# Performance work log

Hardware: AMD Instinct MI355X
Metric: run time of the kernel (lower is better)

The kernel has to match this reference:

```python
import jax, jax.numpy as jnp
import numpy as np

B, S, E, D = 8, 2048, 1024, 512

def setup_inputs() -> dict:
    key = jax.random.key(0)
    ks = jax.random.split(key, 7)
    scale = 1.0 / np.sqrt(E)
    return {
        "X": jax.random.normal(ks[0], (B, S, E), dtype=jnp.float32),
        "lam": jnp.float32(0.8),
        "W_q": jax.random.uniform(ks[1], (E, 2 * D), jnp.float32, -scale, scale),
        "b_q": jax.random.uniform(ks[2], (2 * D,), jnp.float32, -scale, scale),
        "W_k": jax.random.uniform(ks[3], (E, 2 * D), jnp.float32, -scale, scale),
        "b_k": jax.random.uniform(ks[4], (2 * D,), jnp.float32, -scale, scale),
        "W_v": jax.random.uniform(ks[5], (E, D), jnp.float32, -scale, scale),
        "b_v": jax.random.uniform(ks[6], (D,), jnp.float32, -scale, scale),
    }

def reference(X, lam, W_q, b_q, W_k, b_k, W_v, b_v):
    # Projections
    Q = X @ W_q + b_q          # [B, S, 2D]
    K = X @ W_k + b_k          # [B, S, 2D]
    V = X @ W_v + b_v          # [B, S, D]
    Q1, Q2 = Q[..., :D], Q[..., D:]
    K1, K2 = K[..., :D], K[..., D:]
    s = 1.0 / np.sqrt(D)
    A1 = jnp.einsum('bqd,bkd->bqk', Q1, K1) * s  # [B, S, S]
    A2 = jnp.einsum('bqd,bkd->bqk', Q2, K2) * s
    P = jax.nn.softmax(A1, axis=-1) - lam * jax.nn.softmax(A2, axis=-1)
    return jnp.einsum('bqk,bkd->bqd', P, V)      # [B, S, D]
```

## Files before the change

kernel.cpp:

```cpp
#include <hip/hip_runtime.h>


typedef unsigned short u16;
typedef short    bf16x8 __attribute__((ext_vector_type(8)));
typedef unsigned short u16x8 __attribute__((ext_vector_type(8)));
typedef unsigned short u16x4 __attribute__((ext_vector_type(4)));
typedef float    f32x4  __attribute__((ext_vector_type(4)));

typedef __attribute__((address_space(3))) unsigned int       lds_uint;
typedef __attribute__((address_space(1))) const unsigned int gl_uint;

__device__ __forceinline__ void glds16(const void* g, void* l) {
  __builtin_amdgcn_global_load_lds((gl_uint*)g, (lds_uint*)l, 16, 0, 0);
}

__device__ __forceinline__ u16 to_bf16(float f) {
  unsigned u = __float_as_uint(f);
  return (u16)((u + 0x7FFFu + ((u >> 16) & 1u)) >> 16);
}
__device__ __forceinline__ float b2f(u16 h) {
  return __uint_as_float(((unsigned)h) << 16);
}


__global__ void cvt_x(const float4* __restrict__ in, u16x4* __restrict__ out, int n4) {
  int i = blockIdx.x * 256 + threadIdx.x;
  if (i >= n4) return;
  float4 v = in[i];
  u16x4 o;
  o[0] = to_bf16(v.x); o[1] = to_bf16(v.y); o[2] = to_bf16(v.z); o[3] = to_bf16(v.w);
  out[i] = o;
}

__global__ void transpose_cvt(const float* __restrict__ in, u16* __restrict__ out,
                              int R, int C) {
  __shared__ float t[64][65];
  int c0 = blockIdx.x * 64, r0 = blockIdx.y * 64;
  int tx = threadIdx.x, ty = threadIdx.y;
  #pragma unroll
  for (int i = 0; i < 64; i += 4)
    t[ty + i][tx] = in[(long)(r0 + ty + i) * C + c0 + tx];
  __syncthreads();
  #pragma unroll
  for (int i = 0; i < 64; i += 4)
    out[(long)(c0 + ty + i) * R + r0 + tx] = to_bf16(t[tx][ty + i]);
}

__global__ void concat2(const float* __restrict__ a, const float* __restrict__ b,
                        float* __restrict__ o, int n) {
  int i = blockIdx.x * 256 + threadIdx.x;
  if (i < n) o[i] = a[i];
  else if (i < 2 * n) o[i] = b[i - n];
}

__device__ __forceinline__ void swizzle_tiles(int& tm, int& tn) {
  int nx = gridDim.x;
  int lin = blockIdx.y * nx + blockIdx.x;
  int span = nx * 4;
  int group = lin / span;
  int ing = lin % span;
  tm = group * 4 + (ing & 3);
  tn = ing >> 2;
}

__global__ __launch_bounds__(256, 4) void gemm_nt(
    const u16* __restrict__ A, int lda,
    const u16* __restrict__ B, int ldb,
    u16* __restrict__ C1, u16* __restrict__ C2, int splitN, int ldc,
    int Kd, float scale,
    const float* __restrict__ bias, int biasMode)
{
  __shared__ u16 SM[2][8192];
  u16* As = SM[0];
  u16* Bs = SM[1];

  int tid = threadIdx.x;
  int wave = tid >> 6, lane = tid & 63;
  int quad = lane >> 4, ln = lane & 15;
  int wm = wave >> 1, wn = wave & 1;
  int tm, tn;
  swizzle_tiles(tm, tn);
  int c8 = lane >> 3, ml = lane & 7;

  const f32x4 fz = {0.f, 0.f, 0.f, 0.f};
  f32x4 acc[4][4];
  #pragma unroll
  for (int i = 0; i < 4; i++)
    #pragma unroll
    for (int j = 0; j < 4; j++) acc[i][j] = fz;

  const u16* Abase = A + (long)(tm * 128 + ml) * lda + c8 * 8;
  const u16* Bbase = B + (long)(tn * 128 + ml) * ldb + c8 * 8;

  for (int kt = 0; kt < Kd; kt += 64) {
    __syncthreads();
    #pragma unroll
    for (int i = 0; i < 4; i++) {
      int mg = wave * 4 + i;
      glds16(Abase + (long)mg * 8 * lda + kt, &As[mg * 512]);
      glds16(Bbase + (long)mg * 8 * ldb + kt, &Bs[mg * 512]);
    }
    __syncthreads();
    #pragma unroll
    for (int ks = 0; ks < 2; ks++) {
      bf16x8 af[4], bfr[4];
      int c = ks * 4 + quad;
      #pragma unroll
      for (int mt = 0; mt < 4; mt++) {
        int m = wm * 64 + mt * 16 + ln;
        af[mt] = *(const bf16x8*)&As[((m >> 3) * 64 + c * 8 + (m & 7)) * 8];
      }
      #pragma unroll
      for (int nt = 0; nt < 4; nt++) {
        int n = wn * 64 + nt * 16 + ln;
        bfr[nt] = *(const bf16x8*)&Bs[((n >> 3) * 64 + c * 8 + (n & 7)) * 8];
      }
      #pragma unroll
      for (int mt = 0; mt < 4; mt++)
        #pragma unroll
        for (int nt = 0; nt < 4; nt++)
          acc[mt][nt] = __builtin_amdgcn_mfma_f32_16x16x32_bf16(af[mt], bfr[nt], acc[mt][nt], 0, 0, 0);
    }
  }

  int rowBase = tm * 128 + wm * 64;
  int colBase = tn * 128 + wn * 64;
  u16* Cw = C1; int outCol = colBase;
  if (colBase >= splitN) { Cw = C2; outCol = colBase - splitN; }
  u16* eb = &SM[0][0] + wave * 4096;

  __syncthreads();
  #pragma unroll
  for (int mt = 0; mt < 4; mt++) {
    #pragma unroll
    for (int nt = 0; nt < 4; nt++) {
      int colL = nt * 16 + ln;
      float bcol = (biasMode == 1) ? bias[colBase + colL] : 0.f;
      #pragma unroll
      for (int r = 0; r < 4; r++) {
        int rowL = mt * 16 + quad * 4 + r;
        float brow = (biasMode == 2) ? bias[rowBase + rowL] : 0.f;
        float v = acc[mt][nt][r] * scale + bcol + brow;
        eb[rowL * 64 + (((colL >> 3) ^ (rowL & 7)) << 3) + (colL & 7)] = to_bf16(v);
      }
    }
  }
  {
    int row = lane;
    long gr = (long)(rowBase + row) * ldc + outCol;
    #pragma unroll
    for (int c = 0; c < 8; c++) {
      u16x8 ch = *(const u16x8*)&eb[row * 64 + ((c ^ (row & 7)) << 3)];
      *(u16x8*)&Cw[gr + c * 8] = ch;
    }
  }
}


__global__ __launch_bounds__(512, 2) void gemm_s256p(
    const u16* __restrict__ Q, const u16* __restrict__ K,
    u16* __restrict__ E1, u16* __restrict__ E2,
    float* __restrict__ statsP, float scale)
{
  __shared__ u16 SM[73728];

  int bz = blockIdx.z >> 1, half = blockIdx.z & 1;
  const u16* A = Q + (long)bz * 2097152 + half * 512;
  const u16* B = K + (long)bz * 2097152 + half * 512;
  u16* Ed = (half ? E2 : E1) + (long)bz * 4194304;
  float* sp = statsP + (long)blockIdx.z * 65536;

  int tn = blockIdx.x;
  int tmg = blockIdx.y;
  int tid = threadIdx.x;
  int wave = tid >> 6, lane = tid & 63, quad = lane >> 4, ln = lane & 15;
  int wm = wave >> 2, wn = wave & 3;
  int dr = ((lane >> 5) << 3) + (lane & 7);
  int cg = (lane >> 3) & 3;

  const f32x4 fz = {0.f, 0.f, 0.f, 0.f};
  f32x4 acc[8][4];
  #pragma unroll
  for (int i = 0; i < 8; i++)
    #pragma unroll
    for (int j = 0; j < 4; j++) acc[i][j] = fz;

  const u16* Abase = A + (long)(tmg * 1024 + wave * 32 + dr) * 1024 + cg * 8;
  const u16* Bbase = B + (long)(tn * 256 + wave * 32 + dr) * 1024 + cg * 8;
  u16* ldsA0 = SM;
  u16* ldsB0 = SM + 16384;
  u16* eb = SM + 40960 + wave * 4096;

  glds16(Abase,                ldsA0 + wave * 1024);
  glds16(Abase + 16 * 1024,    ldsA0 + wave * 1024 + 512);
  glds16(Bbase,                ldsB0 + wave * 1024);
  glds16(Bbase + 16 * 1024,    ldsB0 + wave * 1024 + 512);
  glds16(Bbase + 32,           ldsB0 + 8192 + wave * 1024);
  glds16(Bbase + 16 * 1024 + 32, ldsB0 + 8192 + wave * 1024 + 512);
  asm volatile("s_waitcnt vmcnt(2)" ::: "memory");
  __builtin_amdgcn_s_barrier();
  __builtin_amdgcn_sched_barrier(0);

  for (int T = 0; T < 64; T++) {
    const u16* Ar = ldsA0 + (T & 1) * 8192;
    const u16* Br = ldsB0 + (T % 3) * 8192;

    {
      int Ta = (T + 1 < 64) ? T + 1 : 63;
      long roff = (long)((Ta >> 4) * 256) * 1024 + ((Ta & 15) << 5);
      u16* dA = ldsA0 + (Ta & 1) * 8192 + wave * 1024;
      glds16(Abase + roff,             dA);
      glds16(Abase + roff + 16 * 1024, dA + 512);
      int Tb = (T + 2 < 64) ? T + 2 : 63;
      int ktB = (Tb & 15) << 5;
      u16* dB = ldsB0 + (Tb % 3) * 8192 + wave * 1024;
      glds16(Bbase + ktB,             dB);
      glds16(Bbase + ktB + 16 * 1024, dB + 512);
    }
    __builtin_amdgcn_sched_barrier(0);

    bf16x8 bfr[4];
    #pragma unroll
    for (int nt = 0; nt < 4; nt++) {
      int n = wn * 64 + nt * 16 + ln;
      bfr[nt] = *(const bf16x8*)(Br + ((n >> 3) * 32 + quad * 8 + (n & 7)) * 8);
    }
    #pragma unroll
    for (int g = 0; g < 8; g++) {
      int m = wm * 128 + g * 16 + ln;
      bf16x8 af = *(const bf16x8*)(Ar + ((m >> 3) * 32 + quad * 8 + (m & 7)) * 8);
      #pragma unroll
      for (int nt = 0; nt < 4; nt++)
        acc[g][nt] = __builtin_amdgcn_mfma_f32_16x16x32_bf16(af, bfr[nt], acc[g][nt], 0, 0, 0);
    }

    asm volatile("s_waitcnt vmcnt(2)" ::: "memory");
    __builtin_amdgcn_s_barrier();
    __builtin_amdgcn_sched_barrier(0);

    if ((T & 15) == 15) {
      int sub = T >> 4;
      int rowBaseW = (tmg * 4 + sub) * 256 + wm * 128;
      int colBase = tn * 256 + wn * 64;
      int kb = tn * 4 + wn;
      #pragma unroll
      for (int h = 0; h < 2; h++) {
        #pragma unroll
        for (int mt = 0; mt < 4; mt++) {
          #pragma unroll
          for (int nt = 0; nt < 4; nt++) {
            int colL = nt * 16 + ln;
            #pragma unroll
            for (int r = 0; r < 4; r++) {
              int rowL = mt * 16 + quad * 4 + r;
              eb[rowL * 64 + (((colL >> 3) ^ (rowL & 7)) << 3) + (colL & 7)] =
                  to_bf16(__expf(acc[h * 4 + mt][nt][r] * scale));
            }
          }
        }
        {
          int row = lane;
          u16x8 ch[8];
          #pragma unroll
          for (int c = 0; c < 8; c++)
            ch[c] = *(const u16x8*)&eb[row * 64 + ((c ^ (row & 7)) << 3)];
          u16* Ep = Ed + (long)(rowBaseW + h * 64 + row) * 2048 + colBase;
          #pragma unroll
          for (int c = 0; c < 8; c++)
            *(u16x8*)&Ep[c * 8] = ch[c];
          float L = 0.f;
          #pragma unroll
          for (int c = 0; c < 8; c++)
            #pragma unroll
            for (int j = 0; j < 8; j++) L += b2f(ch[c][j]);
          sp[(rowBaseW + h * 64 + row) * 32 + kb] = L;
        }
      }
      #pragma unroll
      for (int i = 0; i < 8; i++)
        #pragma unroll
        for (int j = 0; j < 4; j++) acc[i][j] = fz;
    }
  }
  asm volatile("s_waitcnt vmcnt(0)" ::: "memory");
}

__global__ __launch_bounds__(512, 2) void gemm_nt256p(
    const u16* __restrict__ A, const u16* __restrict__ B,
    u16* __restrict__ C1, u16* __restrict__ C2, int splitN, int ldc,
    float scale, const float* __restrict__ bias, int biasMode)
{
  __shared__ u16 SM[73728];

  int tn = blockIdx.x;
  int tmg = blockIdx.y;
  int tid = threadIdx.x;
  int wave = tid >> 6, lane = tid & 63, quad = lane >> 4, ln = lane & 15;
  int wm = wave >> 2, wn = wave & 3;
  int dr = ((lane >> 5) << 3) + (lane & 7);
  int cg = (lane >> 3) & 3;

  const f32x4 fz = {0.f, 0.f, 0.f, 0.f};
  f32x4 acc[8][4];
  #pragma unroll
  for (int i = 0; i < 8; i++)
    #pragma unroll
    for (int j = 0; j < 4; j++) acc[i][j] = fz;

  const u16* Abase = A + (long)(tmg * 512 + wave * 32 + dr) * 1024 + cg * 8;
  const u16* Bbase = B + (long)(tn * 256 + wave * 32 + dr) * 1024 + cg * 8;
  u16* ldsA0 = SM;
  u16* ldsB0 = SM + 16384;
  u16* eb = SM + 40960 + wave * 4096;

  glds16(Abase,                  ldsA0 + wave * 1024);
  glds16(Abase + 16 * 1024,      ldsA0 + wave * 1024 + 512);
  glds16(Bbase,                  ldsB0 + wave * 1024);
  glds16(Bbase + 16 * 1024,      ldsB0 + wave * 1024 + 512);
  glds16(Bbase + 32,             ldsB0 + 8192 + wave * 1024);
  glds16(Bbase + 16 * 1024 + 32, ldsB0 + 8192 + wave * 1024 + 512);
  asm volatile("s_waitcnt vmcnt(2)" ::: "memory");
  __builtin_amdgcn_s_barrier();
  __builtin_amdgcn_sched_barrier(0);

  for (int T = 0; T < 64; T++) {
    const u16* Ar = ldsA0 + (T & 1) * 8192;
    const u16* Br = ldsB0 + (T % 3) * 8192;

    {
      int Ta = (T + 1 < 64) ? T + 1 : 63;
      long roff = (long)((Ta >> 5) * 256) * 1024 + ((Ta & 31) << 5);
      u16* dA = ldsA0 + (Ta & 1) * 8192 + wave * 1024;
      glds16(Abase + roff,             dA);
      glds16(Abase + roff + 16 * 1024, dA + 512);
      int Tb = (T + 2 < 64) ? T + 2 : 63;
      int ktB = (Tb & 31) << 5;
      u16* dB = ldsB0 + (Tb % 3) * 8192 + wave * 1024;
      glds16(Bbase + ktB,             dB);
      glds16(Bbase + ktB + 16 * 1024, dB + 512);
    }
    __builtin_amdgcn_sched_barrier(0);

    bf16x8 bfr[4];
    #pragma unroll
    for (int nt = 0; nt < 4; nt++) {
      int n = wn * 64 + nt * 16 + ln;
      bfr[nt] = *(const bf16x8*)(Br + ((n >> 3) * 32 + quad * 8 + (n & 7)) * 8);
    }
    #pragma unroll
    for (int g = 0; g < 8; g++) {
      int m = wm * 128 + g * 16 + ln;
      bf16x8 af = *(const bf16x8*)(Ar + ((m >> 3) * 32 + quad * 8 + (m & 7)) * 8);
      #pragma unroll
      for (int nt = 0; nt < 4; nt++)
        acc[g][nt] = __builtin_amdgcn_mfma_f32_16x16x32_bf16(af, bfr[nt], acc[g][nt], 0, 0, 0);
    }

    asm volatile("s_waitcnt vmcnt(2)" ::: "memory");
    __builtin_amdgcn_s_barrier();
    __builtin_amdgcn_sched_barrier(0);

    if ((T & 31) == 31) {
      int sub = T >> 5;
      int rowBaseW = (tmg * 2 + sub) * 256 + wm * 128;
      int colBase = tn * 256 + wn * 64;
      u16* Cw = C1; int outCol = colBase;
      if (colBase >= splitN) { Cw = C2; outCol = colBase - splitN; }
      #pragma unroll
      for (int h = 0; h < 2; h++) {
        #pragma unroll
        for (int mt = 0; mt < 4; mt++) {
          #pragma unroll
          for (int nt = 0; nt < 4; nt++) {
            int colL = nt * 16 + ln;
            float bcol = (biasMode == 1) ? bias[colBase + colL] : 0.f;
            #pragma unroll
            for (int r = 0; r < 4; r++) {
              int rowL = mt * 16 + quad * 4 + r;
              float brow = (biasMode == 2) ? bias[rowBaseW + h * 64 + rowL] : 0.f;
              float v = acc[h * 4 + mt][nt][r] * scale + bcol + brow;
              eb[rowL * 64 + (((colL >> 3) ^ (rowL & 7)) << 3) + (colL & 7)] = to_bf16(v);
            }
          }
        }
        {
          int row = lane;
          long gr = (long)(rowBaseW + h * 64 + row) * ldc + outCol;
          #pragma unroll
          for (int c = 0; c < 8; c++) {
            u16x8 ch = *(const u16x8*)&eb[row * 64 + ((c ^ (row & 7)) << 3)];
            *(u16x8*)&Cw[gr + c * 8] = ch;
          }
        }
      }
      #pragma unroll
      for (int i = 0; i < 8; i++)
        #pragma unroll
        for (int j = 0; j < 4; j++) acc[i][j] = fz;
    }
  }
  asm volatile("s_waitcnt vmcnt(0)" ::: "memory");
}

__global__ void stats_reduce(const float* __restrict__ sp, float* __restrict__ so,
                             const float* __restrict__ lamPtr) {
  int gid = blockIdx.x * 256 + threadIdx.x;
  const float* p = sp + (long)gid * 32;
  float L = 0.f;
  #pragma unroll
  for (int kb = 0; kb < 32; kb++) L += p[kb];
  int half = (gid >> 11) & 1;
  so[gid] = (half ? lamPtr[0] : 1.0f) / L;
}

__global__ __launch_bounds__(512, 2) void apply_pv(
    const u16* __restrict__ E1, const u16* __restrict__ E2,
    const u16* __restrict__ VT, const float* __restrict__ inv,
    float* __restrict__ Out)
{
  __shared__ u16 Vs[2][32768];
  __shared__ u16 Pb[2][4096];
  __shared__ float i1s[64], i2s[64];

  const int NT = 32;
  int b = blockIdx.x & 7, qt = blockIdx.x >> 3;
  int q0 = qt * 64;
  int tid = threadIdx.x;
  int wave = tid >> 6, lane = tid & 63, quad = lane >> 4, ln = lane & 15;
  int c8 = lane >> 3, ml = lane & 7;
  int r = tid >> 3, cg8 = tid & 7;

  const u16* e1p = E1 + ((long)b * 2048 + q0 + r) * 2048 + cg8 * 8;
  const u16* e2p = E2 + ((long)b * 2048 + q0 + r) * 2048 + cg8 * 8;
  const u16* Vbase = VT + (long)b * 2048;
  int pw = (r >> 3) * 512 + cg8 * 64 + (r & 7) * 8;

  const f32x4 fz = {0.f, 0.f, 0.f, 0.f};
  f32x4 acc[4][4];
  #pragma unroll
  for (int i = 0; i < 4; i++)
    #pragma unroll
    for (int j = 0; j < 4; j++) acc[i][j] = fz;

  if (tid < 64)       i1s[tid]       = inv[(long)(b * 2 + 0) * 2048 + q0 + tid];
  else if (tid < 128) i2s[tid - 64]  = inv[(long)(b * 2 + 1) * 2048 + q0 + (tid - 64)];
  u16x8 a1 = *(const u16x8*)(e1p);
  u16x8 a2 = *(const u16x8*)(e2p);
  __builtin_amdgcn_sched_barrier(0);
  #pragma unroll
  for (int i = 0; i < 8; i++) {
    int dg = wave * 8 + i;
    glds16(Vbase + (long)(dg * 8 + ml) * 16384 + c8 * 8, &Vs[0][dg * 512]);
  }
  __builtin_amdgcn_sched_barrier(0);
  asm volatile("s_waitcnt lgkmcnt(0)" ::: "memory");
  __builtin_amdgcn_s_barrier();
  __builtin_amdgcn_sched_barrier(0);
  float i1 = i1s[r], i2 = i2s[r];
  {
    u16x8 o;
    #pragma unroll
    for (int j = 0; j < 8; j++)
      o[j] = to_bf16(b2f(a1[j]) * i1 - b2f(a2[j]) * i2);
    *(u16x8*)&Pb[0][pw] = o;
  }
  a1 = *(const u16x8*)(e1p + 64);
  a2 = *(const u16x8*)(e2p + 64);
  __builtin_amdgcn_sched_barrier(0);
  asm volatile("s_waitcnt lgkmcnt(0)" ::: "memory");
  asm volatile("s_waitcnt vmcnt(2)" ::: "memory");
  __builtin_amdgcn_sched_barrier(0);
  __builtin_amdgcn_s_barrier();
  __builtin_amdgcn_sched_barrier(0);

  for (int t = 0; t < NT; t++) {
    const int p = t & 1;
    const u16* Vr = &Vs[p][0];
    const u16* Pr = &Pb[p][0];
    u16* Vw = &Vs[p ^ 1][0];
    u16* Pw = &Pb[p ^ 1][0];
    int ktv = ((t + 1 < NT) ? (t + 1) : (NT - 1)) << 6;
    int kte = ((t + 2 < NT) ? (t + 2) : (NT - 1)) << 6;
    bf16x8 vf[2][4];

    #pragma unroll
    for (int q = 0; q < 4; q++) {
      bf16x8 pf[2];
      #pragma unroll
      for (int ks = 0; ks < 2; ks++) {
        int m = q * 16 + ln;
        pf[ks] = *(const bf16x8*)&Pr[((m >> 3) * 64 + (ks * 4 + quad) * 8 + (m & 7)) * 8];
      }
      if (q == 0) {
        #pragma unroll
        for (int ks = 0; ks < 2; ks++)
          #pragma unroll
          for (int nt = 0; nt < 4; nt++) {
            int d = wave * 64 + nt * 16 + ln;
            vf[ks][nt] = *(const bf16x8*)&Vr[((d >> 3) * 64 + (ks * 4 + quad) * 8 + (d & 7)) * 8];
          }
      }
      #pragma unroll
      for (int i = 0; i < 2; i++) {
        int dg = wave * 8 + q * 2 + i;
        glds16(Vbase + (long)(dg * 8 + ml) * 16384 + ktv + c8 * 8, Vw + dg * 512);
      }
      if (q == 3) {
        __builtin_amdgcn_sched_barrier(0);
        u16x8 o;
        #pragma unroll
        for (int j = 0; j < 8; j++)
          o[j] = to_bf16(b2f(a1[j]) * i1 - b2f(a2[j]) * i2);
        *(u16x8*)&Pw[pw] = o;
        a1 = *(const u16x8*)(e1p + kte);
        a2 = *(const u16x8*)(e2p + kte);
      }
      __builtin_amdgcn_sched_barrier(0);
      __builtin_amdgcn_s_barrier();
      asm volatile("s_waitcnt lgkmcnt(0)" ::: "memory");
      __builtin_amdgcn_sched_barrier(0);
      __builtin_amdgcn_s_setprio(1);
      #pragma unroll
      for (int ks = 0; ks < 2; ks++)
        #pragma unroll
        for (int nt = 0; nt < 4; nt++)
          acc[q][nt] = __builtin_amdgcn_mfma_f32_16x16x32_bf16(pf[ks], vf[ks][nt], acc[q][nt], 0, 0, 0);
      __builtin_amdgcn_s_setprio(0);
      __builtin_amdgcn_sched_barrier(0);
      if (q == 3) asm volatile("s_waitcnt vmcnt(2)" ::: "memory");
      __builtin_amdgcn_s_barrier();
      __builtin_amdgcn_sched_barrier(0);
    }
  }

  #pragma unroll
  for (int mt = 0; mt < 4; mt++)
    #pragma unroll
    for (int nt = 0; nt < 4; nt++)
      #pragma unroll
      for (int r2 = 0; r2 < 4; r2++)
        Out[((long)b * 2048 + q0 + mt * 16 + quad * 4 + r2) * 512 + wave * 64 + nt * 16 + ln] =
            acc[mt][nt][r2];
}


extern "C" void kernel_launch(void* const* d_in, const int* in_sizes, int n_in,
                              void* d_out, int out_size, void* d_ws, size_t ws_size,
                              hipStream_t stream)
{
  const float* X   = (const float*)d_in[0];
  const float* lam = (const float*)d_in[1];
  const float* Wq  = (const float*)d_in[2];
  const float* bq  = (const float*)d_in[3];
  const float* Wk  = (const float*)d_in[4];
  const float* bk  = (const float*)d_in[5];
  const float* Wv  = (const float*)d_in[6];
  const float* bv  = (const float*)d_in[7];
  float* Out = (float*)d_out;
  char* ws = (char*)d_ws;

  u16*  WqkT   = (u16*)(ws + 0);
  u16*  WvT    = (u16*)(ws + 4194304);
  float* bqk   = (float*)(ws + 5242880);
  u16*  Qb     = (u16*)(ws + 6291456);
  u16*  Kb     = (u16*)(ws + 39845888);
  u16*  VTb    = (u16*)(ws + 73400320);
  u16*  Xb     = (u16*)(ws + 90177536);
  u16*  E1     = (u16*)(ws + 90177536);
  u16*  E2     = (u16*)(ws + 157286400);
  float* statsP= (float*)(ws + 224395264);
  float* invD  = (float*)(ws + 228589568);

  cvt_x<<<16384, 256, 0, stream>>>((const float4*)X, (u16x4*)Xb, 4194304);
  transpose_cvt<<<dim3(16, 16), dim3(64, 4), 0, stream>>>(Wq, WqkT, 1024, 1024);
  transpose_cvt<<<dim3(16, 16), dim3(64, 4), 0, stream>>>(Wk, WqkT + 1024 * 1024, 1024, 1024);
  transpose_cvt<<<dim3(8, 16),  dim3(64, 4), 0, stream>>>(Wv, WvT, 1024, 512);
  concat2<<<8, 256, 0, stream>>>(bq, bk, bqk, 1024);

  gemm_nt256p<<<dim3(8, 32), 512, 0, stream>>>(Xb, WqkT, Qb, Kb, 1024, 1024,
                                               1.0f, bqk, 1);
  gemm_nt<<<dim3(128, 4), 256, 0, stream>>>(WvT, 1024, Xb, 1024,
                                            VTb, VTb, 1 << 30, 16384,
                                            1024, 1.0f, bv, 2);

  const float s = 0.044194173824159216f;
  gemm_s256p<<<dim3(8, 2, 16), 512, 0, stream>>>(Qb, Kb, E1, E2, statsP, s);

  stats_reduce<<<128, 256, 0, stream>>>(statsP, invD, lam);
  apply_pv<<<256, 512, 0, stream>>>(E1, E2, VTb, invD, Out);
}
```

Before: 474.9 us.

## Shrink QK and score GEMM tiles to 128x128 with grouped block swizzle

The Q/K projection GEMM and the score GEMM move from 512-thread blocks with 256x256 tiles and a triple-buffered B pipeline to 256-thread blocks with 128x128 tiles, double buffering and 40KB LDS. Blocks are launched as a flat grid remapped into groups of eight panels for L2 locality. The aim is more resident blocks per CU and more blocks in the grid for better load balance. In exchange each tile gets less operand reuse and has to wait on vmcnt(0) every step, removing the prefetch depth. The epilogue now writes 16-row chunks and uses shuffles to reduce the row sums.

```diff
diff --git a/kernel.cpp b/kernel.cpp
--- a/kernel.cpp
+++ b/kernel.cpp
@@ -157,65 +157,67 @@
 }
 
 
-__global__ __launch_bounds__(512, 2) void gemm_s256p(
+__global__ __launch_bounds__(256, 4) void gemm_s128p(
     const u16* __restrict__ Q, const u16* __restrict__ K,
     u16* __restrict__ E1, u16* __restrict__ E2,
     float* __restrict__ statsP, float scale)
 {
-  __shared__ u16 SM[73728];
-
-  int bz = blockIdx.z >> 1, half = blockIdx.z & 1;
+  __shared__ u16 SM[20480];
+
+  int blk = blockIdx.x;
+  int g = blk & 7, r = blk >> 3;
+  int pan = g + 8 * (r >> 4);
+  int tn = r & 15;
+  int tmg = pan & 3, z = pan >> 2;
+  int bz = z >> 1, half = z & 1;
+
   const u16* A = Q + (long)bz * 2097152 + half * 512;
   const u16* B = K + (long)bz * 2097152 + half * 512;
   u16* Ed = (half ? E2 : E1) + (long)bz * 4194304;
-  float* sp = statsP + (long)blockIdx.z * 65536;
-
-  int tn = blockIdx.x;
-  int tmg = blockIdx.y;
+  float* sp = statsP + (long)z * 65536;
+
   int tid = threadIdx.x;
   int wave = tid >> 6, lane = tid & 63, quad = lane >> 4, ln = lane & 15;
-  int wm = wave >> 2, wn = wave & 3;
+  int wm = wave >> 1, wn = wave & 1;
   int dr = ((lane >> 5) << 3) + (lane & 7);
   int cg = (lane >> 3) & 3;
 
   const f32x4 fz = {0.f, 0.f, 0.f, 0.f};
-  f32x4 acc[8][4];
-  #pragma unroll
-  for (int i = 0; i < 8; i++)
+  f32x4 acc[4][4];
+  #pragma unroll
+  for (int i = 0; i < 4; i++)
     #pragma unroll
     for (int j = 0; j < 4; j++) acc[i][j] = fz;
 
-  const u16* Abase = A + (long)(tmg * 1024 + wave * 32 + dr) * 1024 + cg * 8;
-  const u16* Bbase = B + (long)(tn * 256 + wave * 32 + dr) * 1024 + cg * 8;
-  u16* ldsA0 = SM;
-  u16* ldsB0 = SM + 16384;
-  u16* eb = SM + 40960 + wave * 4096;
-
-  glds16(Abase,                ldsA0 + wave * 1024);
-  glds16(Abase + 16 * 1024,    ldsA0 + wave * 1024 + 512);
-  glds16(Bbase,                ldsB0 + wave * 1024);
-  glds16(Bbase + 16 * 1024,    ldsB0 + wave * 1024 + 512);
-  glds16(Bbase + 32,           ldsB0 + 8192 + wave * 1024);
-  glds16(Bbase + 16 * 1024 + 32, ldsB0 + 8192 + wave * 1024 + 512);
-  asm volatile("s_waitcnt vmcnt(2)" ::: "memory");
+  const u16* Ab = A + (long)(tmg * 512 + dr) * 1024 + cg * 8;
+  const u16* Bb = B + (long)(tn * 128 + dr) * 1024 + cg * 8;
+  u16* eb = SM + 16384 + wave * 1024;
+
+  #pragma unroll
+  for (int i = 0; i < 2; i++) {
+    int g16 = wave * 2 + i;
+    glds16(Ab + (long)(g16 * 16) * 1024, SM + g16 * 512);
+    glds16(Bb + (long)(g16 * 16) * 1024, SM + 8192 + g16 * 512);
+  }
+  asm volatile("s_waitcnt vmcnt(0)" ::: "memory");
   __builtin_amdgcn_s_barrier();
   __builtin_amdgcn_sched_barrier(0);
 
   for (int T = 0; T < 64; T++) {
-    const u16* Ar = ldsA0 + (T & 1) * 8192;
-    const u16* Br = ldsB0 + (T % 3) * 8192;
+    const u16* Ar = SM + (T & 1) * 4096;
+    const u16* Br = SM + 8192 + (T & 1) * 4096;
 
     {
-      int Ta = (T + 1 < 64) ? T + 1 : 63;
-      long roff = (long)((Ta >> 4) * 256) * 1024 + ((Ta & 15) << 5);
-      u16* dA = ldsA0 + (Ta & 1) * 8192 + wave * 1024;
-      glds16(Abase + roff,             dA);
-      glds16(Abase + roff + 16 * 1024, dA + 512);
-      int Tb = (T + 2 < 64) ? T + 2 : 63;
-      int ktB = (Tb & 15) << 5;
-      u16* dB = ldsB0 + (Tb % 3) * 8192 + wave * 1024;
-      glds16(Bbase + ktB,             dB);
-      glds16(Bbase + ktB + 16 * 1024, dB + 512);
+      int Tn = (T + 1 < 64) ? T + 1 : 63;
+      int sub_n = Tn >> 4, kt_n = (Tn & 15) << 5;
+      u16* dA = SM + (Tn & 1) * 4096;
+      u16* dB = SM + 8192 + (Tn & 1) * 4096;
+      #pragma unroll
+      for (int i = 0; i < 2; i++) {
+        int g16 = wave * 2 + i;
+        glds16(Ab + (long)(sub_n * 128 + g16 * 16) * 1024 + kt_n, dA + g16 * 512);
+        glds16(Bb + (long)(g16 * 16) * 1024 + kt_n,               dB + g16 * 512);
+      }
     }
     __builtin_amdgcn_sched_barrier(0);
 
@@ -223,121 +225,119 @@
     #pragma unroll
     for (int nt = 0; nt < 4; nt++) {
       int n = wn * 64 + nt * 16 + ln;
-      bfr[nt] = *(const bf16x8*)(Br + ((n >> 3) * 32 + quad * 8 + (n & 7)) * 8);
-    }
-    #pragma unroll
-    for (int g = 0; g < 8; g++) {
-      int m = wm * 128 + g * 16 + ln;
-      bf16x8 af = *(const bf16x8*)(Ar + ((m >> 3) * 32 + quad * 8 + (m & 7)) * 8);
+      bfr[nt] = *(const bf16x8*)(Br + (n >> 3) * 256 + quad * 64 + (n & 7) * 8);
+    }
+    #pragma unroll
+    for (int mt = 0; mt < 4; mt++) {
+      int m = wm * 64 + mt * 16 + ln;
+      bf16x8 af = *(const bf16x8*)(Ar + (m >> 3) * 256 + quad * 64 + (m & 7) * 8);
       #pragma unroll
       for (int nt = 0; nt < 4; nt++)
-        acc[g][nt] = __builtin_amdgcn_mfma_f32_16x16x32_bf16(af, bfr[nt], acc[g][nt], 0, 0, 0);
-    }
-
-    asm volatile("s_waitcnt vmcnt(2)" ::: "memory");
+        acc[mt][nt] = __builtin_amdgcn_mfma_f32_16x16x32_bf16(af, bfr[nt], acc[mt][nt], 0, 0, 0);
+    }
+
+    asm volatile("s_waitcnt vmcnt(0)" ::: "memory");
     __builtin_amdgcn_s_barrier();
     __builtin_amdgcn_sched_barrier(0);
 
     if ((T & 15) == 15) {
       int sub = T >> 4;
-      int rowBaseW = (tmg * 4 + sub) * 256 + wm * 128;
-      int colBase = tn * 256 + wn * 64;
-      int kb = tn * 4 + wn;
-      #pragma unroll
-      for (int h = 0; h < 2; h++) {
-        #pragma unroll
-        for (int mt = 0; mt < 4; mt++) {
+      int rowB = tmg * 512 + sub * 128 + wm * 64;
+      int colB = tn * 128 + wn * 64;
+      int kb = tn * 2 + wn;
+      #pragma unroll
+      for (int c2 = 0; c2 < 4; c2++) {
+        #pragma unroll
+        for (int nt = 0; nt < 4; nt++) {
+          int colL = nt * 16 + ln;
           #pragma unroll
-          for (int nt = 0; nt < 4; nt++) {
-            int colL = nt * 16 + ln;
-            #pragma unroll
-            for (int r = 0; r < 4; r++) {
-              int rowL = mt * 16 + quad * 4 + r;
-              eb[rowL * 64 + (((colL >> 3) ^ (rowL & 7)) << 3) + (colL & 7)] =
-                  to_bf16(__expf(acc[h * 4 + mt][nt][r] * scale));
-            }
+          for (int rr = 0; rr < 4; rr++) {
+            int rowL = quad * 4 + rr;
+            eb[rowL * 64 + (((colL >> 3) ^ (rowL & 7)) << 3) + (colL & 7)] =
+                to_bf16(__expf(acc[c2][nt][rr] * scale));
           }
         }
         {
-          int row = lane;
-          u16x8 ch[8];
+          int row = lane & 15, hf = lane >> 4;
+          float L = 0.f;
+          u16x8 ch[2];
           #pragma unroll
-          for (int c = 0; c < 8; c++)
-            ch[c] = *(const u16x8*)&eb[row * 64 + ((c ^ (row & 7)) << 3)];
-          u16* Ep = Ed + (long)(rowBaseW + h * 64 + row) * 2048 + colBase;
-          #pragma unroll
-          for (int c = 0; c < 8; c++)
-            *(u16x8*)&Ep[c * 8] = ch[c];
-          float L = 0.f;
-          #pragma unroll
-          for (int c = 0; c < 8; c++)
+          for (int cc = 0; cc < 2; cc++) {
+            int c = hf * 2 + cc;
+            ch[cc] = *(const u16x8*)&eb[row * 64 + ((c ^ (row & 7)) << 3)];
             #pragma unroll
-            for (int j = 0; j < 8; j++) L += b2f(ch[c][j]);
-          sp[(rowBaseW + h * 64 + row) * 32 + kb] = L;
+            for (int j = 0; j < 8; j++) L += b2f(ch[cc][j]);
+          }
+          u16* Ep = Ed + (long)(rowB + c2 * 16 + row) * 2048 + colB + hf * 16;
+          *(u16x8*)&Ep[0] = ch[0];
+          *(u16x8*)&Ep[8] = ch[1];
+          L += __shfl_xor(L, 16);
+          L += __shfl_xor(L, 32);
+          if (hf == 0)
+            sp[(rowB + c2 * 16 + row) * 32 + kb] = L;
         }
-      }
-      #pragma unroll
-      for (int i = 0; i < 8; i++)
-        #pragma unroll
-        for (int j = 0; j < 4; j++) acc[i][j] = fz;
+        #pragma unroll
+        for (int j = 0; j < 4; j++) acc[c2][j] = fz;
+      }
     }
   }
   asm volatile("s_waitcnt vmcnt(0)" ::: "memory");
 }
 
-__global__ __launch_bounds__(512, 2) void gemm_nt256p(
+__global__ __launch_bounds__(256, 4) void gemm_nt128p(
     const u16* __restrict__ A, const u16* __restrict__ B,
     u16* __restrict__ C1, u16* __restrict__ C2, int splitN, int ldc,
-    float scale, const float* __restrict__ bias, int biasMode)
+    const float* __restrict__ bias)
 {
-  __shared__ u16 SM[73728];
-
-  int tn = blockIdx.x;
-  int tmg = blockIdx.y;
+  __shared__ u16 SM[20480];
+
+  int blk = blockIdx.x;
+  int g = blk & 7, r = blk >> 3;
+  int pan = g + 8 * (r >> 4);
+  int tn = r & 15;
+
   int tid = threadIdx.x;
   int wave = tid >> 6, lane = tid & 63, quad = lane >> 4, ln = lane & 15;
-  int wm = wave >> 2, wn = wave & 3;
+  int wm = wave >> 1, wn = wave & 1;
   int dr = ((lane >> 5) << 3) + (lane & 7);
   int cg = (lane >> 3) & 3;
 
   const f32x4 fz = {0.f, 0.f, 0.f, 0.f};
-  f32x4 acc[8][4];
-  #pragma unroll
-  for (int i = 0; i < 8; i++)
+  f32x4 acc[4][4];
+  #pragma unroll
+  for (int i = 0; i < 4; i++)
     #pragma unroll
     for (int j = 0; j < 4; j++) acc[i][j] = fz;
 
-  const u16* Abase = A + (long)(tmg * 512 + wave * 32 + dr) * 1024 + cg * 8;
-  const u16* Bbase = B + (long)(tn * 256 + wave * 32 + dr) * 1024 + cg * 8;
-  u16* ldsA0 = SM;
-  u16* ldsB0 = SM + 16384;
-  u16* eb = SM + 40960 + wave * 4096;
-
-  glds16(Abase,                  ldsA0 + wave * 1024);
-  glds16(Abase + 16 * 1024,      ldsA0 + wave * 1024 + 512);
-  glds16(Bbase,                  ldsB0 + wave * 1024);
-  glds16(Bbase + 16 * 1024,      ldsB0 + wave * 1024 + 512);
-  glds16(Bbase + 32,             ldsB0 + 8192 + wave * 1024);
-  glds16(Bbase + 16 * 1024 + 32, ldsB0 + 8192 + wave * 1024 + 512);
-  asm volatile("s_waitcnt vmcnt(2)" ::: "memory");
+  const u16* Ab = A + (long)(pan * 256 + dr) * 1024 + cg * 8;
+  const u16* Bb = B + (long)(tn * 128 + dr) * 1024 + cg * 8;
+  u16* eb = SM + 16384 + wave * 1024;
+
+  #pragma unroll
+  for (int i = 0; i < 2; i++) {
+    int g16 = wave * 2 + i;
+    glds16(Ab + (long)(g16 * 16) * 1024, SM + g16 * 512);
+    glds16(Bb + (long)(g16 * 16) * 1024, SM + 8192 + g16 * 512);
+  }
+  asm volatile("s_waitcnt vmcnt(0)" ::: "memory");
   __builtin_amdgcn_s_barrier();
   __builtin_amdgcn_sched_barrier(0);
 
   for (int T = 0; T < 64; T++) {
-    const u16* Ar = ldsA0 + (T & 1) * 8192;
-    const u16* Br = ldsB0 + (T % 3) * 8192;
+    const u16* Ar = SM + (T & 1) * 4096;
+    const u16* Br = SM + 8192 + (T & 1) * 4096;
 
     {
-      int Ta = (T + 1 < 64) ? T + 1 : 63;
-      long roff = (long)((Ta >> 5) * 256) * 1024 + ((Ta & 31) << 5);
-      u16* dA = ldsA0 + (Ta & 1) * 8192 + wave * 1024;
-      glds16(Abase + roff,             dA);
-      glds16(Abase + roff + 16 * 1024, dA + 512);
-      int Tb = (T + 2 < 64) ? T + 2 : 63;
-      int ktB = (Tb & 31) << 5;
-      u16* dB = ldsB0 + (Tb % 3) * 8192 + wave * 1024;
-      glds16(Bbase + ktB,             dB);
-      glds16(Bbase + ktB + 16 * 1024, dB + 512);
+      int Tn = (T + 1 < 64) ? T + 1 : 63;
+      int sub_n = Tn >> 5, kt_n = (Tn & 31) << 5;
+      u16* dA = SM + (Tn & 1) * 4096;
+      u16* dB = SM + 8192 + (Tn & 1) * 4096;
+      #pragma unroll
+      for (int i = 0; i < 2; i++) {
+        int g16 = wave * 2 + i;
+        glds16(Ab + (long)(sub_n * 128 + g16 * 16) * 1024 + kt_n, dA + g16 * 512);
+        glds16(Bb + (long)(g16 * 16) * 1024 + kt_n,               dB + g16 * 512);
+      }
     }
     __builtin_amdgcn_sched_barrier(0);
 
@@ -345,58 +345,55 @@
     #pragma unroll
     for (int nt = 0; nt < 4; nt++) {
       int n = wn * 64 + nt * 16 + ln;
-      bfr[nt] = *(const bf16x8*)(Br + ((n >> 3) * 32 + quad * 8 + (n & 7)) * 8);
-    }
-    #pragma unroll
-    for (int g = 0; g < 8; g++) {
-      int m = wm * 128 + g * 16 + ln;
-      bf16x8 af = *(const bf16x8*)(Ar + ((m >> 3) * 32 + quad * 8 + (m & 7)) * 8);
+      bfr[nt] = *(const bf16x8*)(Br + (n >> 3) * 256 + quad * 64 + (n & 7) * 8);
+    }
+    #pragma unroll
+    for (int mt = 0; mt < 4; mt++) {
+      int m = wm * 64 + mt * 16 + ln;
+      bf16x8 af = *(const bf16x8*)(Ar + (m >> 3) * 256 + quad * 64 + (m & 7) * 8);
       #pragma unroll
       for (int nt = 0; nt < 4; nt++)
-        acc[g][nt] = __builtin_amdgcn_mfma_f32_16x16x32_bf16(af, bfr[nt], acc[g][nt], 0, 0, 0);
-    }
-
-    asm volatile("s_waitcnt vmcnt(2)" ::: "memory");
+        acc[mt][nt] = __builtin_amdgcn_mfma_f32_16x16x32_bf16(af, bfr[nt], acc[mt][nt], 0, 0, 0);
+    }
+
+    asm volatile("s_waitcnt vmcnt(0)" ::: "memory");
     __builtin_amdgcn_s_barrier();
     __builtin_amdgcn_sched_barrier(0);
 
     if ((T & 31) == 31) {
       int sub = T >> 5;
-      int rowBaseW = (tmg * 2 + sub) * 256 + wm * 128;
-      int colBase = tn * 256 + wn * 64;
-      u16* Cw = C1; int outCol = colBase;
-      if (colBase >= splitN) { Cw = C2; outCol = colBase - splitN; }
-      #pragma unroll
-      for (int h = 0; h < 2; h++) {
-        #pragma unroll
-        for (int mt = 0; mt < 4; mt++) {
+      int rowB = pan * 256 + sub * 128 + wm * 64;
+      int colB = tn * 128 + wn * 64;
+      u16* Cw = C1; int outCol = colB;
+      if (colB >= splitN) { Cw = C2; outCol = colB - splitN; }
+      #pragma unroll
+      for (int c2 = 0; c2 < 4; c2++) {
+        #pragma unroll
+        for (int nt = 0; nt < 4; nt++) {
+          int colL = nt * 16 + ln;
+          float bcol = bias[colB + colL];
           #pragma unroll
-          for (int nt = 0; nt < 4; nt++) {
-            int colL = nt * 16 + ln;
-            float bcol = (biasMode == 1) ? bias[colBase + colL] : 0.f;
-            #pragma unroll
-            for (int r = 0; r < 4; r++) {
-              int rowL = mt * 16 + quad * 4 + r;
-              float brow = (biasMode == 2) ? bias[rowBaseW + h * 64 + rowL] : 0.f;
-              float v = acc[h * 4 + mt][nt][r] * scale + bcol + brow;
-              eb[rowL * 64 + (((colL >> 3) ^ (rowL & 7)) << 3) + (colL & 7)] = to_bf16(v);
-            }
+          for (int rr = 0; rr < 4; rr++) {
+            int rowL = quad * 4 + rr;
+            eb[rowL * 64 + (((colL >> 3) ^ (rowL & 7)) << 3) + (colL & 7)] =
+                to_bf16(acc[c2][nt][rr] + bcol);
           }
         }
         {
-          int row = lane;
-          long gr = (long)(rowBaseW + h * 64 + row) * ldc + outCol;
+          int row = lane & 15, hf = lane >> 4;
+          u16x8 ch[2];
           #pragma unroll
-          for (int c = 0; c < 8; c++) {
-            u16x8 ch = *(const u16x8*)&eb[row * 64 + ((c ^ (row & 7)) << 3)];
-            *(u16x8*)&Cw[gr + c * 8] = ch;
+          for (int cc = 0; cc < 2; cc++) {
+            int c = hf * 2 + cc;
+            ch[cc] = *(const u16x8*)&eb[row * 64 + ((c ^ (row & 7)) << 3)];
           }
+          long gr = (long)(rowB + c2 * 16 + row) * ldc + outCol + hf * 16;
+          *(u16x8*)&Cw[gr]     = ch[0];
+          *(u16x8*)&Cw[gr + 8] = ch[1];
         }
-      }
-      #pragma unroll
-      for (int i = 0; i < 8; i++)
-        #pragma unroll
-        for (int j = 0; j < 4; j++) acc[i][j] = fz;
+        #pragma unroll
+        for (int j = 0; j < 4; j++) acc[c2][j] = fz;
+      }
     }
   }
   asm volatile("s_waitcnt vmcnt(0)" ::: "memory");
@@ -577,14 +574,13 @@
   transpose_cvt<<<dim3(8, 16),  dim3(64, 4), 0, stream>>>(Wv, WvT, 1024, 512);
   concat2<<<8, 256, 0, stream>>>(bq, bk, bqk, 1024);
 
-  gemm_nt256p<<<dim3(8, 32), 512, 0, stream>>>(Xb, WqkT, Qb, Kb, 1024, 1024,
-                                               1.0f, bqk, 1);
+  gemm_nt128p<<<1024, 256, 0, stream>>>(Xb, WqkT, Qb, Kb, 1024, 1024, bqk);
   gemm_nt<<<dim3(128, 4), 256, 0, stream>>>(WvT, 1024, Xb, 1024,
                                             VTb, VTb, 1 << 30, 16384,
                                             1024, 1.0f, bv, 2);
 
   const float s = 0.044194173824159216f;
-  gemm_s256p<<<dim3(8, 2, 16), 512, 0, stream>>>(Qb, Kb, E1, E2, statsP, s);
+  gemm_s128p<<<1024, 256, 0, stream>>>(Qb, Kb, E1, E2, statsP, s);
 
   stats_reduce<<<128, 256, 0, stream>>>(statsP, invD, lam);
   apply_pv<<<256, 512, 0, stream>>>(E1, E2, VTb, invD, Out);
```

New measurement: 535.6 us. 1.13x slower.
